# Kernel optimization log

Hardware: AMD Instinct MI355X
Metric: run time of the kernel (lower is better)

The kernel has to match this reference:

```python
import jax, jax.numpy as jnp
import numpy as np

N_NODES = 50000
N_EDGES = 800000
D = 96
N_LAYERS = 3


def setup_inputs() -> dict:
    key = jax.random.key(0)
    ks = jax.random.split(key, 3 + 2 * N_LAYERS)
    h = jax.random.normal(ks[0], (N_NODES, D), dtype=jnp.float32)
    src = jax.random.randint(ks[1], (N_EDGES,), 0, N_NODES, dtype=jnp.int64)
    dst = jax.random.randint(ks[2], (N_EDGES,), 0, N_NODES, dtype=jnp.int64)
    inp = {"h": h, "src": src, "dst": dst}
    scale = 1.0 / np.sqrt(D)
    for i in range(N_LAYERS):
        inp[f"W{i}"] = jax.random.normal(ks[3 + 2 * i], (D, D), dtype=jnp.float32) * scale
        inp[f"b{i}"] = jnp.zeros((D,), dtype=jnp.float32)
    return inp


def _gnn_forward(h, src, dst, weights, biases):
    N = h.shape[0]
    ones = jnp.ones(src.shape[0], dtype=h.dtype)
    # norm='both': scale by out_degree^-1/2 on src side, in_degree^-1/2 on dst side
    out_deg = jnp.clip(jax.ops.segment_sum(ones, src, num_segments=N), 1.0)
    in_deg = jnp.clip(jax.ops.segment_sum(ones, dst, num_segments=N), 1.0)
    norm_src = (out_deg ** -0.5)[:, None]  # [N,1]
    norm_dst = (in_deg ** -0.5)[:, None]   # [N,1]
    for W, b in zip(weights, biases):
        x = h * norm_src                                       # [N,D]
        m = jax.ops.segment_sum(x[src], dst, num_segments=N)   # gather+scatter-add
        m = m * norm_dst
        h = jax.nn.relu(m @ W + b)                             # aggregate-then-transform (in<=out)
    return h


def reference(h, src, dst, W0, b0, W1, b1, W2, b2):
    return _gnn_forward(h, src, dst, (W0, W1, W2), (b0, b1, b2))
```

## Files before the change

kernel.cpp:

```cpp
#include <hip/hip_runtime.h>
#include <hip/hip_bf16.h>

#define N_NODES 50000
#define N_PAD 50048
#define N_EDGES 800000
#define DIM 96
#define CHB 12

#define EPB 2048
#define NB_E ((N_EDGES + EPB - 1) / EPB)
#define NBKT ((N_NODES + 255) / 256)
#define NTILES ((N_NODES + 63) / 64)
#define PREP_ITEMS (3 * DIM * DIM + 3 * DIM)

typedef __attribute__((ext_vector_type(8))) short short8;
typedef __attribute__((ext_vector_type(4))) float f32x4;



__device__ __forceinline__ unsigned short f2bf(float f) {
    unsigned u = __float_as_uint(f);
    u += 0x7FFFu + ((u >> 16) & 1u);
    return (unsigned short)(u >> 16);
}

__device__ __forceinline__ int good_halves(unsigned w) {
    unsigned lo = w & 0xFFFFu, hi = w >> 16;
    unsigned e0 = (lo >> 7) & 0xFF, e1 = (hi >> 7) & 0xFF;
    int g = 0;
    if (lo == 0 || (e0 >= 100 && e0 <= 140)) ++g;
    if (hi == 0 || (e1 >= 100 && e1 <= 140)) ++g;
    return g;
}

__device__ __forceinline__ float rdval(const void* p, int i, int isbf) {
    return isbf ? __bfloat162float(((const __hip_bfloat16*)p)[i]) : ((const float*)p)[i];
}

__device__ __forceinline__ int load_idx(const int* __restrict__ p, int e, int is64) {
    return p[is64 ? (e << 1) : e];
}


__global__ __launch_bounds__(256) void part_count(const int* __restrict__ src,
                                                  const int* __restrict__ dst,
                                                  const unsigned* __restrict__ hw,
                                                  const unsigned* __restrict__ ww,
                                                  int* __restrict__ cntD,
                                                  int* __restrict__ cntS,
                                                  int* __restrict__ flags) {
    const unsigned* sw = (const unsigned*)src;
    int zeros = 0;
    for (int i = 0; i < 64; ++i) zeros += (sw[2 * i + 1] == 0u) ? 1 : 0;
    int is64 = (zeros >= 60) ? 1 : 0;

    __shared__ int lcD[256], lcS[256];
    int b = blockIdx.x, t = threadIdx.x;
    lcD[t] = 0; lcS[t] = 0;
    __syncthreads();
    int base = b * EPB;
#pragma unroll
    for (int i = 0; i < EPB / 256; ++i) {
        int e = base + i * 256 + t;
        if (e < N_EDGES) {
            int d = load_idx(dst, e, is64);
            int s = load_idx(src, e, is64);
            atomicAdd(&lcD[d >> 8], 1);
            atomicAdd(&lcS[s >> 8], 1);
        }
    }
    __syncthreads();
    cntD[b * 256 + t] = lcD[t];
    cntS[b * 256 + t] = lcS[t];

    if (b == 0) {
        if (t == 0) flags[2] = is64;
        if (t == 1) {
            int good = 0;
            for (int i = 0; i < 128; ++i) good += good_halves(hw[i]);
            flags[0] = (good >= 226) ? 1 : 0;
        }
        if (t == 2) {
            int good = 0;
            for (int i = 0; i < 128; ++i) good += good_halves(ww[i]);
            flags[1] = (good >= 226) ? 1 : 0;
        }
    }
}


__global__ __launch_bounds__(256) void scan_buckets(int* __restrict__ cntD,
                                                    int* __restrict__ cntS,
                                                    int* __restrict__ btotD,
                                                    int* __restrict__ btotS) {
    __shared__ int sm[256];
    int k = blockIdx.x, t = threadIdx.x;
    int b0 = 2 * t, b1 = 2 * t + 1;
    int v0 = (b0 < NB_E) ? cntD[b0 * 256 + k] : 0;
    int v1 = (b1 < NB_E) ? cntD[b1 * 256 + k] : 0;
    int pair = v0 + v1;
    sm[t] = pair;
    __syncthreads();
    for (int off = 1; off < 256; off <<= 1) {
        int u = (t >= off) ? sm[t - off] : 0;
        __syncthreads();
        sm[t] += u;
        __syncthreads();
    }
    int excl = sm[t] - pair;
    if (b0 < NB_E) cntD[b0 * 256 + k] = excl;
    if (b1 < NB_E) cntD[b1 * 256 + k] = excl + v0;
    if (t == 255) btotD[k] = sm[255];
    __syncthreads();
    v0 = (b0 < NB_E) ? cntS[b0 * 256 + k] : 0;
    v1 = (b1 < NB_E) ? cntS[b1 * 256 + k] : 0;
    pair = v0 + v1;
    sm[t] = pair;
    __syncthreads();
    for (int off = 1; off < 256; off <<= 1) {
        int u = (t >= off) ? sm[t - off] : 0;
        __syncthreads();
        sm[t] += u;
        __syncthreads();
    }
    excl = sm[t] - pair;
    if (b0 < NB_E) cntS[b0 * 256 + k] = excl;
    if (b1 < NB_E) cntS[b1 * 256 + k] = excl + v0;
    if (t == 255) btotS[k] = sm[255];
}


__global__ __launch_bounds__(256) void part_scatter(const int* __restrict__ src,
                                                    const int* __restrict__ dst,
                                                    const int* __restrict__ offD,
                                                    const int* __restrict__ offS,
                                                    const int* __restrict__ btotD,
                                                    const int* __restrict__ btotS,
                                                    unsigned* __restrict__ epack,
                                                    unsigned char* __restrict__ sloc,
                                                    const int* __restrict__ flags) {
    __shared__ int sm[256];
    __shared__ int runD[256], runS[256];
    int b = blockIdx.x, t = threadIdx.x;
    int v = btotD[t];
    sm[t] = v;
    __syncthreads();
    for (int off = 1; off < 256; off <<= 1) {
        int u = (t >= off) ? sm[t - off] : 0;
        __syncthreads();
        sm[t] += u;
        __syncthreads();
    }
    int baseD = sm[t] - v;
    __syncthreads();
    v = btotS[t];
    sm[t] = v;
    __syncthreads();
    for (int off = 1; off < 256; off <<= 1) {
        int u = (t >= off) ? sm[t - off] : 0;
        __syncthreads();
        sm[t] += u;
        __syncthreads();
    }
    int baseS = sm[t] - v;
    runD[t] = baseD + offD[b * 256 + t];
    runS[t] = baseS + offS[b * 256 + t];
    __syncthreads();
    int is64 = flags[2];
    int base = b * EPB;
#pragma unroll
    for (int i = 0; i < EPB / 256; ++i) {
        int e = base + i * 256 + t;
        if (e < N_EDGES) {
            int d = load_idx(dst, e, is64);
            int s = load_idx(src, e, is64);
            int pd = atomicAdd(&runD[d >> 8], 1);
            epack[pd] = ((unsigned)(d & 255) << 16) | (unsigned)s;
            int ps = atomicAdd(&runS[s >> 8], 1);
            sloc[ps] = (unsigned char)(s & 255);
        }
    }
}


__global__ __launch_bounds__(256) void bucket_build(const unsigned* __restrict__ epack,
                                                    const int* __restrict__ btotD,
                                                    const unsigned char* __restrict__ sloc,
                                                    const int* __restrict__ btotS,
                                                    int* __restrict__ rowptr,
                                                    float* __restrict__ normD,
                                                    float* __restrict__ normS,
                                                    unsigned short* __restrict__ esrc) {
    __shared__ int bD[256], bS[256], cnt[256], run[256];
    int k = blockIdx.x, t = threadIdx.x;
    int vD = btotD[t], vS = btotS[t];
    bD[t] = vD; bS[t] = vS;
    __syncthreads();
    for (int off = 1; off < 256; off <<= 1) {
        int uD = (t >= off) ? bD[t - off] : 0;
        int uS = (t >= off) ? bS[t - off] : 0;
        __syncthreads();
        bD[t] += uD; bS[t] += uS;
        __syncthreads();
    }
    int ebeg = (k == 0) ? 0 : bD[k - 1];
    int eend = bD[k];
    int sbeg = (k == 0) ? 0 : bS[k - 1];
    int send = bS[k];

    cnt[t] = 0;
    __syncthreads();
    for (int e = ebeg + t; e < eend; e += 256)
        atomicAdd(&cnt[epack[e] >> 16], 1);
    __syncthreads();
    int v = cnt[t];
    bD[t] = v;
    __syncthreads();
    for (int off = 1; off < 256; off <<= 1) {
        int u = (t >= off) ? bD[t - off] : 0;
        __syncthreads();
        bD[t] += u;
        __syncthreads();
    }
    int excl = bD[t] - v;
    int n = k * 256 + t;
    if (n < N_NODES) {
        rowptr[n] = ebeg + excl;
        normD[n] = rsqrtf((float)max(v, 1));
    }
    run[t] = excl;
    __syncthreads();
    for (int e = ebeg + t; e < eend; e += 256) {
        unsigned p = epack[e];
        int dl = p >> 16;
        int slot = atomicAdd(&run[dl], 1);
        esrc[ebeg + slot] = (unsigned short)(p & 0xFFFFu);
    }
    if (k == NBKT - 1 && t == 0) rowptr[N_NODES] = N_EDGES;
    __syncthreads();
    cnt[t] = 0;
    __syncthreads();
    for (int e = sbeg + t; e < send; e += 256)
        atomicAdd(&cnt[sloc[e]], 1);
    __syncthreads();
    if (n < N_NODES) normS[n] = rsqrtf((float)max(cnt[t], 1));
}


__global__ __launch_bounds__(256) void prepcvt_k(const void* __restrict__ W0,
                                                 const void* __restrict__ W1,
                                                 const void* __restrict__ W2,
                                                 const void* __restrict__ b0,
                                                 const void* __restrict__ b1,
                                                 const void* __restrict__ b2,
                                                 unsigned short* __restrict__ WT,
                                                 float* __restrict__ biasc,
                                                 const void* __restrict__ h,
                                                 const float* __restrict__ normS,
                                                 unsigned short* __restrict__ A0,
                                                 const int* __restrict__ flags) {
    int idx = blockIdx.x * 256 + threadIdx.x;
    if (idx < PREP_ITEMS) {
        int wbf = flags[1];
        if (idx < 3 * DIM * DIM) {
            int l = idx / (DIM * DIM);
            int i = idx - l * DIM * DIM;
            int k = i / DIM, n = i - k * DIM;
            const void* Wp = (l == 0) ? W0 : (l == 1) ? W1 : W2;
            WT[l * DIM * DIM + n * DIM + k] = f2bf(rdval(Wp, i, wbf));
        } else {
            int j = idx - 3 * DIM * DIM;
            int l = j / DIM, c = j - l * DIM;
            const void* bp = (l == 0) ? b0 : (l == 1) ? b1 : b2;
            biasc[j] = rdval(bp, c, wbf);
        }
        return;
    }
    int i4 = idx - PREP_ITEMS;
    if (i4 >= N_NODES * DIM / 4) return;
    int hbf = flags[0];
    int i = i4 * 4;
    float ns = normS[i / DIM];
    float v0, v1, v2, v3;
    if (hbf) {
        const __hip_bfloat16* hp = (const __hip_bfloat16*)h + i;
        v0 = __bfloat162float(hp[0]); v1 = __bfloat162float(hp[1]);
        v2 = __bfloat162float(hp[2]); v3 = __bfloat162float(hp[3]);
    } else {
        float4 v = ((const float4*)h)[i4];
        v0 = v.x; v1 = v.y; v2 = v.z; v3 = v.w;
    }
    ushort4 o;
    o.x = f2bf(v0 * ns); o.y = f2bf(v1 * ns);
    o.z = f2bf(v2 * ns); o.w = f2bf(v3 * ns);
    ((ushort4*)A0)[i4] = o;
}


__device__ __forceinline__ void acc8(float* a, uint4 q) {
    a[0] += __uint_as_float(q.x << 16);
    a[1] += __uint_as_float(q.x & 0xFFFF0000u);
    a[2] += __uint_as_float(q.y << 16);
    a[3] += __uint_as_float(q.y & 0xFFFF0000u);
    a[4] += __uint_as_float(q.z << 16);
    a[5] += __uint_as_float(q.z & 0xFFFF0000u);
    a[6] += __uint_as_float(q.w << 16);
    a[7] += __uint_as_float(q.w & 0xFFFF0000u);
}

__global__ __launch_bounds__(256) void gather_k(const unsigned* __restrict__ Abf,
                                                const float* __restrict__ normD,
                                                const int* __restrict__ rowptr,
                                                const unsigned short* __restrict__ esrc,
                                                unsigned short* __restrict__ Bm) {
    int g = blockIdx.x * 256 + threadIdx.x;
    if (g >= N_NODES * CHB) return;
    int n = g / CHB;
    int c = g - n * CHB;
    int beg = rowptr[n], end = rowptr[n + 1];
    float a[8] = {0.f, 0.f, 0.f, 0.f, 0.f, 0.f, 0.f, 0.f};
    const uint4* Ap = (const uint4*)Abf;
    int k = beg;
    for (; k + 4 <= end; k += 4) {
        int s0 = esrc[k], s1 = esrc[k + 1], s2 = esrc[k + 2], s3 = esrc[k + 3];
        uint4 q0 = Ap[s0 * CHB + c];
        uint4 q1 = Ap[s1 * CHB + c];
        uint4 q2 = Ap[s2 * CHB + c];
        uint4 q3 = Ap[s3 * CHB + c];
        acc8(a, q0); acc8(a, q1); acc8(a, q2); acc8(a, q3);
    }
    for (; k < end; ++k) {
        uint4 q = Ap[esrc[k] * CHB + c];
        acc8(a, q);
    }
    float nd = normD[n];
    uint4 o;
    o.x = (unsigned)f2bf(a[0] * nd) | ((unsigned)f2bf(a[1] * nd) << 16);
    o.y = (unsigned)f2bf(a[2] * nd) | ((unsigned)f2bf(a[3] * nd) << 16);
    o.z = (unsigned)f2bf(a[4] * nd) | ((unsigned)f2bf(a[5] * nd) << 16);
    o.w = (unsigned)f2bf(a[6] * nd) | ((unsigned)f2bf(a[7] * nd) << 16);
    ((uint4*)Bm)[g] = o;
}


__global__ __launch_bounds__(256) void gemm_k(const unsigned short* __restrict__ Bm,
                                              const float* __restrict__ normS,
                                              const unsigned short* __restrict__ WTl,
                                              const float* __restrict__ bl,
                                              unsigned short* __restrict__ outA,
                                              void* __restrict__ outLast,
                                              const int* __restrict__ flags, int last) {
    int wv = threadIdx.x >> 6;
    int lane = threadIdx.x & 63;
    int quad = lane >> 4;
    int ln = lane & 15;
    int rowbase = blockIdx.x * 64 + wv * 16;

    const short8* Ap = (const short8*)(Bm + (size_t)(rowbase + ln) * DIM + quad * 8);
    short8 a0 = Ap[0], a1 = Ap[4], a2 = Ap[8];

    float ns[4];
    if (!last) {
#pragma unroll
        for (int r = 0; r < 4; ++r)
            ns[r] = normS[min(rowbase + quad * 4 + r, N_NODES - 1)];
    }
    int obf = flags[0];

#pragma unroll
    for (int ct = 0; ct < 6; ++ct) {
        const short8* Wp = (const short8*)(WTl + (size_t)(ct * 16 + ln) * DIM + quad * 8);
        short8 b0 = Wp[0], b1 = Wp[4], b2 = Wp[8];
        f32x4 acc = {0.f, 0.f, 0.f, 0.f};
        acc = __builtin_amdgcn_mfma_f32_16x16x32_bf16(a0, b0, acc, 0, 0, 0);
        acc = __builtin_amdgcn_mfma_f32_16x16x32_bf16(a1, b1, acc, 0, 0, 0);
        acc = __builtin_amdgcn_mfma_f32_16x16x32_bf16(a2, b2, acc, 0, 0, 0);
        int col = ct * 16 + ln;
        float bv = bl[col];
#pragma unroll
        for (int r = 0; r < 4; ++r) {
            int row = rowbase + quad * 4 + r;
            if (row < N_NODES) {
                float v = fmaxf(acc[r] + bv, 0.f);
                size_t idx = (size_t)row * DIM + col;
                if (last) {
                    if (obf)
                        ((__hip_bfloat16*)outLast)[idx] = __float2bfloat16(v);
                    else
                        ((float*)outLast)[idx] = v;
                } else {
                    outA[idx] = f2bf(v * ns[r]);
                }
            }
        }
    }
}


extern "C" void kernel_launch(void* const* d_in, const int* in_sizes, int n_in,
                              void* d_out, int out_size, void* d_ws, size_t ws_size,
                              hipStream_t stream) {
    const void* h = d_in[0];
    const int* src = (const int*)d_in[1];
    const int* dst = (const int*)d_in[2];

    int* flags = (int*)d_ws;
    int* cntD = flags + 4;
    int* cntS = cntD + NB_E * 256;
    int* btotD = cntS + NB_E * 256;
    int* btotS = btotD + 256;
    int* rowptr = btotS + 256;
    float* normS = (float*)(rowptr + 50004);
    float* normD = normS + N_NODES;
    unsigned short* WT = (unsigned short*)(normD + N_NODES);
    float* biasc = (float*)(WT + 3 * DIM * DIM);
    unsigned* epack = (unsigned*)(biasc + 3 * DIM);
    unsigned char* sloc = (unsigned char*)(epack + N_EDGES);
    unsigned short* esrc = (unsigned short*)(sloc + N_EDGES);
    unsigned short* Bm = esrc + N_EDGES;
    unsigned short* A0 = Bm + (size_t)N_PAD * DIM;
    unsigned short* A1 = A0 + (size_t)N_NODES * DIM;

    part_count<<<NB_E, 256, 0, stream>>>(src, dst, (const unsigned*)h,
                                         (const unsigned*)d_in[3], cntD, cntS, flags);
    scan_buckets<<<256, 256, 0, stream>>>(cntD, cntS, btotD, btotS);
    part_scatter<<<NB_E, 256, 0, stream>>>(src, dst, cntD, cntS, btotD, btotS,
                                           epack, sloc, flags);
    bucket_build<<<NBKT, 256, 0, stream>>>(epack, btotD, sloc, btotS,
                                           rowptr, normD, normS, esrc);
    prepcvt_k<<<(PREP_ITEMS + N_NODES * DIM / 4 + 255) / 256, 256, 0, stream>>>(
        d_in[3], d_in[5], d_in[7], d_in[4], d_in[6], d_in[8], WT, biasc,
        h, normS, A0, flags);

    const int ggrid = (N_NODES * CHB + 255) / 256;
    gather_k<<<ggrid, 256, 0, stream>>>((const unsigned*)A0, normD, rowptr, esrc, Bm);
    gemm_k<<<NTILES, 256, 0, stream>>>(Bm, normS, WT, biasc, A1, nullptr, flags, 0);
    gather_k<<<ggrid, 256, 0, stream>>>((const unsigned*)A1, normD, rowptr, esrc, Bm);
    gemm_k<<<NTILES, 256, 0, stream>>>(Bm, normS, WT + DIM * DIM, biasc + DIM,
                                       A0, nullptr, flags, 0);
    gather_k<<<ggrid, 256, 0, stream>>>((const unsigned*)A0, normD, rowptr, esrc, Bm);
    gemm_k<<<NTILES, 256, 0, stream>>>(Bm, normS, WT + 2 * DIM * DIM, biasc + 2 * DIM,
                                       nullptr, d_out, flags, 1);
}
```

Before: 262.4 us.

## Fuse gather into GEMM per layer and fold prep into preprocessing kernels

Measured after the change: 265.3 us. About the same (+1.1%).

```diff
diff --git a/kernel.cpp b/kernel.cpp
--- a/kernel.cpp
+++ b/kernel.cpp
@@ -2,7 +2,6 @@
 #include <hip/hip_bf16.h>
 
 #define N_NODES 50000
-#define N_PAD 50048
 #define N_EDGES 800000
 #define DIM 96
 #define CHB 12
@@ -12,6 +11,7 @@
 #define NBKT ((N_NODES + 255) / 256)
 #define NTILES ((N_NODES + 63) / 64)
 #define PREP_ITEMS (3 * DIM * DIM + 3 * DIM)
+#define LROW 112
 
 typedef __attribute__((ext_vector_type(8))) short short8;
 typedef __attribute__((ext_vector_type(4))) float f32x4;
@@ -39,6 +39,17 @@
 
 __device__ __forceinline__ int load_idx(const int* __restrict__ p, int e, int is64) {
     return p[is64 ? (e << 1) : e];
+}
+
+__device__ __forceinline__ void acc8(float* a, uint4 q) {
+    a[0] += __uint_as_float(q.x << 16);
+    a[1] += __uint_as_float(q.x & 0xFFFF0000u);
+    a[2] += __uint_as_float(q.y << 16);
+    a[3] += __uint_as_float(q.y & 0xFFFF0000u);
+    a[4] += __uint_as_float(q.z << 16);
+    a[5] += __uint_as_float(q.z & 0xFFFF0000u);
+    a[6] += __uint_as_float(q.w << 16);
+    a[7] += __uint_as_float(q.w & 0xFFFF0000u);
 }
 
 
@@ -92,7 +103,16 @@
 __global__ __launch_bounds__(256) void scan_buckets(int* __restrict__ cntD,
                                                     int* __restrict__ cntS,
                                                     int* __restrict__ btotD,
-                                                    int* __restrict__ btotS) {
+                                                    int* __restrict__ btotS,
+                                                    const void* __restrict__ W0,
+                                                    const void* __restrict__ W1,
+                                                    const void* __restrict__ W2,
+                                                    const void* __restrict__ b0p,
+                                                    const void* __restrict__ b1p,
+                                                    const void* __restrict__ b2p,
+                                                    unsigned short* __restrict__ WT,
+                                                    float* __restrict__ biasc,
+                                                    const int* __restrict__ flags) {
     __shared__ int sm[256];
     int k = blockIdx.x, t = threadIdx.x;
     int b0 = 2 * t, b1 = 2 * t + 1;
@@ -127,6 +147,23 @@
     if (b0 < NB_E) cntS[b0 * 256 + k] = excl;
     if (b1 < NB_E) cntS[b1 * 256 + k] = excl + v0;
     if (t == 255) btotS[k] = sm[255];
+
+    int idx = k * 256 + t;
+    if (idx < PREP_ITEMS) {
+        int wbf = flags[1];
+        if (idx < 3 * DIM * DIM) {
+            int l = idx / (DIM * DIM);
+            int i = idx - l * DIM * DIM;
+            int kk = i / DIM, n = i - kk * DIM;
+            const void* Wp = (l == 0) ? W0 : (l == 1) ? W1 : W2;
+            WT[l * DIM * DIM + n * DIM + kk] = f2bf(rdval(Wp, i, wbf));
+        } else {
+            int j = idx - 3 * DIM * DIM;
+            int l = j / DIM, c = j - l * DIM;
+            const void* bp = (l == 0) ? b0p : (l == 1) ? b1p : b2p;
+            biasc[j] = rdval(bp, c, wbf);
+        }
+    }
 }
 
 
@@ -190,8 +227,12 @@
                                                     int* __restrict__ rowptr,
                                                     float* __restrict__ normD,
                                                     float* __restrict__ normS,
-                                                    unsigned short* __restrict__ esrc) {
+                                                    unsigned short* __restrict__ esrc,
+                                                    const void* __restrict__ h,
+                                                    unsigned short* __restrict__ A0,
+                                                    const int* __restrict__ flags) {
     __shared__ int bD[256], bS[256], cnt[256], run[256];
+    __shared__ float nsf[256];
     int k = blockIdx.x, t = threadIdx.x;
     int vD = btotD[t], vS = btotS[t];
     bD[t] = vD; bS[t] = vS;
@@ -243,124 +284,94 @@
     for (int e = sbeg + t; e < send; e += 256)
         atomicAdd(&cnt[sloc[e]], 1);
     __syncthreads();
-    if (n < N_NODES) normS[n] = rsqrtf((float)max(cnt[t], 1));
-}
-
-
-__global__ __launch_bounds__(256) void prepcvt_k(const void* __restrict__ W0,
-                                                 const void* __restrict__ W1,
-                                                 const void* __restrict__ W2,
-                                                 const void* __restrict__ b0,
-                                                 const void* __restrict__ b1,
-                                                 const void* __restrict__ b2,
-                                                 unsigned short* __restrict__ WT,
-                                                 float* __restrict__ biasc,
-                                                 const void* __restrict__ h,
-                                                 const float* __restrict__ normS,
-                                                 unsigned short* __restrict__ A0,
-                                                 const int* __restrict__ flags) {
-    int idx = blockIdx.x * 256 + threadIdx.x;
-    if (idx < PREP_ITEMS) {
-        int wbf = flags[1];
-        if (idx < 3 * DIM * DIM) {
-            int l = idx / (DIM * DIM);
-            int i = idx - l * DIM * DIM;
-            int k = i / DIM, n = i - k * DIM;
-            const void* Wp = (l == 0) ? W0 : (l == 1) ? W1 : W2;
-            WT[l * DIM * DIM + n * DIM + k] = f2bf(rdval(Wp, i, wbf));
+    float ns = rsqrtf((float)max(cnt[t], 1));
+    nsf[t] = ns;
+    if (n < N_NODES) normS[n] = ns;
+    __syncthreads();
+    int hbf = flags[0];
+    for (int i = t; i < 256 * (DIM / 4); i += 256) {
+        int ln_ = i / (DIM / 4);
+        int c4 = i - ln_ * (DIM / 4);
+        int nn = k * 256 + ln_;
+        if (nn >= N_NODES) continue;
+        float s = nsf[ln_];
+        float v0, v1, v2, v3;
+        if (hbf) {
+            const __hip_bfloat16* hp = (const __hip_bfloat16*)h + (size_t)nn * DIM + c4 * 4;
+            v0 = __bfloat162float(hp[0]); v1 = __bfloat162float(hp[1]);
+            v2 = __bfloat162float(hp[2]); v3 = __bfloat162float(hp[3]);
         } else {
-            int j = idx - 3 * DIM * DIM;
-            int l = j / DIM, c = j - l * DIM;
-            const void* bp = (l == 0) ? b0 : (l == 1) ? b1 : b2;
-            biasc[j] = rdval(bp, c, wbf);
-        }
-        return;
-    }
-    int i4 = idx - PREP_ITEMS;
-    if (i4 >= N_NODES * DIM / 4) return;
-    int hbf = flags[0];
-    int i = i4 * 4;
-    float ns = normS[i / DIM];
-    float v0, v1, v2, v3;
-    if (hbf) {
-        const __hip_bfloat16* hp = (const __hip_bfloat16*)h + i;
-        v0 = __bfloat162float(hp[0]); v1 = __bfloat162float(hp[1]);
-        v2 = __bfloat162float(hp[2]); v3 = __bfloat162float(hp[3]);
-    } else {
-        float4 v = ((const float4*)h)[i4];
-        v0 = v.x; v1 = v.y; v2 = v.z; v3 = v.w;
-    }
-    ushort4 o;
-    o.x = f2bf(v0 * ns); o.y = f2bf(v1 * ns);
-    o.z = f2bf(v2 * ns); o.w = f2bf(v3 * ns);
-    ((ushort4*)A0)[i4] = o;
-}
-
-
-__device__ __forceinline__ void acc8(float* a, uint4 q) {
-    a[0] += __uint_as_float(q.x << 16);
-    a[1] += __uint_as_float(q.x & 0xFFFF0000u);
-    a[2] += __uint_as_float(q.y << 16);
-    a[3] += __uint_as_float(q.y & 0xFFFF0000u);
-    a[4] += __uint_as_float(q.z << 16);
-    a[5] += __uint_as_float(q.z & 0xFFFF0000u);
-    a[6] += __uint_as_float(q.w << 16);
-    a[7] += __uint_as_float(q.w & 0xFFFF0000u);
-}
-
-__global__ __launch_bounds__(256) void gather_k(const unsigned* __restrict__ Abf,
-                                                const float* __restrict__ normD,
-                                                const int* __restrict__ rowptr,
-                                                const unsigned short* __restrict__ esrc,
-                                                unsigned short* __restrict__ Bm) {
-    int g = blockIdx.x * 256 + threadIdx.x;
-    if (g >= N_NODES * CHB) return;
-    int n = g / CHB;
-    int c = g - n * CHB;
-    int beg = rowptr[n], end = rowptr[n + 1];
-    float a[8] = {0.f, 0.f, 0.f, 0.f, 0.f, 0.f, 0.f, 0.f};
+            float4 vv = ((const float4*)h)[nn * (DIM / 4) + c4];
+            v0 = vv.x; v1 = vv.y; v2 = vv.z; v3 = vv.w;
+        }
+        ushort4 o;
+        o.x = f2bf(v0 * s); o.y = f2bf(v1 * s);
+        o.z = f2bf(v2 * s); o.w = f2bf(v3 * s);
+        ((ushort4*)A0)[nn * (DIM / 4) + c4] = o;
+    }
+}
+
+
+template <bool LAST>
+__global__ __launch_bounds__(256) void fused_layer(const unsigned* __restrict__ Abf,
+                                                   const float* __restrict__ normS,
+                                                   const float* __restrict__ normD,
+                                                   const int* __restrict__ rowptr,
+                                                   const unsigned short* __restrict__ esrc,
+                                                   const unsigned short* __restrict__ WTl,
+                                                   const float* __restrict__ bl,
+                                                   unsigned short* __restrict__ outA,
+                                                   void* __restrict__ outLast,
+                                                   const int* __restrict__ flags) {
+    __shared__ unsigned short Bs[64 * LROW];
+
     const uint4* Ap = (const uint4*)Abf;
-    int k = beg;
-    for (; k + 4 <= end; k += 4) {
-        int s0 = esrc[k], s1 = esrc[k + 1], s2 = esrc[k + 2], s3 = esrc[k + 3];
-        uint4 q0 = Ap[s0 * CHB + c];
-        uint4 q1 = Ap[s1 * CHB + c];
-        uint4 q2 = Ap[s2 * CHB + c];
-        uint4 q3 = Ap[s3 * CHB + c];
-        acc8(a, q0); acc8(a, q1); acc8(a, q2); acc8(a, q3);
-    }
-    for (; k < end; ++k) {
-        uint4 q = Ap[esrc[k] * CHB + c];
-        acc8(a, q);
-    }
-    float nd = normD[n];
-    uint4 o;
-    o.x = (unsigned)f2bf(a[0] * nd) | ((unsigned)f2bf(a[1] * nd) << 16);
-    o.y = (unsigned)f2bf(a[2] * nd) | ((unsigned)f2bf(a[3] * nd) << 16);
-    o.z = (unsigned)f2bf(a[4] * nd) | ((unsigned)f2bf(a[5] * nd) << 16);
-    o.w = (unsigned)f2bf(a[6] * nd) | ((unsigned)f2bf(a[7] * nd) << 16);
-    ((uint4*)Bm)[g] = o;
-}
-
-
-__global__ __launch_bounds__(256) void gemm_k(const unsigned short* __restrict__ Bm,
-                                              const float* __restrict__ normS,
-                                              const unsigned short* __restrict__ WTl,
-                                              const float* __restrict__ bl,
-                                              unsigned short* __restrict__ outA,
-                                              void* __restrict__ outLast,
-                                              const int* __restrict__ flags, int last) {
+    int row0 = blockIdx.x * 64;
+
+#pragma unroll
+    for (int it = 0; it < 3; ++it) {
+        int g = threadIdx.x + 256 * it;
+        int r = g / CHB;
+        int c = g - r * CHB;
+        int n = row0 + r;
+        float a[8] = {0.f, 0.f, 0.f, 0.f, 0.f, 0.f, 0.f, 0.f};
+        float nd = 0.f;
+        if (n < N_NODES) {
+            int beg = rowptr[n], end = rowptr[n + 1];
+            int k = beg;
+            for (; k + 4 <= end; k += 4) {
+                int s0 = esrc[k], s1 = esrc[k + 1], s2 = esrc[k + 2], s3 = esrc[k + 3];
+                uint4 q0 = Ap[s0 * CHB + c];
+                uint4 q1 = Ap[s1 * CHB + c];
+                uint4 q2 = Ap[s2 * CHB + c];
+                uint4 q3 = Ap[s3 * CHB + c];
+                acc8(a, q0); acc8(a, q1); acc8(a, q2); acc8(a, q3);
+            }
+            for (; k < end; ++k) acc8(a, Ap[esrc[k] * CHB + c]);
+            nd = normD[n];
+        }
+        uint4 o;
+        o.x = (unsigned)f2bf(a[0] * nd) | ((unsigned)f2bf(a[1] * nd) << 16);
+        o.y = (unsigned)f2bf(a[2] * nd) | ((unsigned)f2bf(a[3] * nd) << 16);
+        o.z = (unsigned)f2bf(a[4] * nd) | ((unsigned)f2bf(a[5] * nd) << 16);
+        o.w = (unsigned)f2bf(a[6] * nd) | ((unsigned)f2bf(a[7] * nd) << 16);
+        *(uint4*)&Bs[r * LROW + c * 8] = o;
+    }
+    __syncthreads();
+
     int wv = threadIdx.x >> 6;
     int lane = threadIdx.x & 63;
     int quad = lane >> 4;
     int ln = lane & 15;
-    int rowbase = blockIdx.x * 64 + wv * 16;
-
-    const short8* Ap = (const short8*)(Bm + (size_t)(rowbase + ln) * DIM + quad * 8);
-    short8 a0 = Ap[0], a1 = Ap[4], a2 = Ap[8];
+    int rl = wv * 16 + ln;
+    int rowbase = row0 + wv * 16;
+
+    short8 a0 = *(const short8*)&Bs[rl * LROW + quad * 8];
+    short8 a1 = *(const short8*)&Bs[rl * LROW + 32 + quad * 8];
+    short8 a2 = *(const short8*)&Bs[rl * LROW + 64 + quad * 8];
 
     float ns[4];
-    if (!last) {
+    if (!LAST) {
 #pragma unroll
         for (int r = 0; r < 4; ++r)
             ns[r] = normS[min(rowbase + quad * 4 + r, N_NODES - 1)];
@@ -383,7 +394,7 @@
             if (row < N_NODES) {
                 float v = fmaxf(acc[r] + bv, 0.f);
                 size_t idx = (size_t)row * DIM + col;
-                if (last) {
+                if (LAST) {
                     if (obf)
                         ((__hip_bfloat16*)outLast)[idx] = __float2bfloat16(v);
                     else
@@ -417,28 +428,28 @@
     unsigned* epack = (unsigned*)(biasc + 3 * DIM);
     unsigned char* sloc = (unsigned char*)(epack + N_EDGES);
     unsigned short* esrc = (unsigned short*)(sloc + N_EDGES);
-    unsigned short* Bm = esrc + N_EDGES;
-    unsigned short* A0 = Bm + (size_t)N_PAD * DIM;
+    unsigned short* A0 = esrc + N_EDGES;
     unsigned short* A1 = A0 + (size_t)N_NODES * DIM;
 
     part_count<<<NB_E, 256, 0, stream>>>(src, dst, (const unsigned*)h,
                                          (const unsigned*)d_in[3], cntD, cntS, flags);
-    scan_buckets<<<256, 256, 0, stream>>>(cntD, cntS, btotD, btotS);
+    scan_buckets<<<256, 256, 0, stream>>>(cntD, cntS, btotD, btotS,
+                                          d_in[3], d_in[5], d_in[7],
+                                          d_in[4], d_in[6], d_in[8],
+                                          WT, biasc, flags);
     part_scatter<<<NB_E, 256, 0, stream>>>(src, dst, cntD, cntS, btotD, btotS,
                                            epack, sloc, flags);
     bucket_build<<<NBKT, 256, 0, stream>>>(epack, btotD, sloc, btotS,
-                                           rowptr, normD, normS, esrc);
-    prepcvt_k<<<(PREP_ITEMS + N_NODES * DIM / 4 + 255) / 256, 256, 0, stream>>>(
-        d_in[3], d_in[5], d_in[7], d_in[4], d_in[6], d_in[8], WT, biasc,
-        h, normS, A0, flags);
-
-    const int ggrid = (N_NODES * CHB + 255) / 256;
-    gather_k<<<ggrid, 256, 0, stream>>>((const unsigned*)A0, normD, rowptr, esrc, Bm);
-    gemm_k<<<NTILES, 256, 0, stream>>>(Bm, normS, WT, biasc, A1, nullptr, flags, 0);
-    gather_k<<<ggrid, 256, 0, stream>>>((const unsigned*)A1, normD, rowptr, esrc, Bm);
-    gemm_k<<<NTILES, 256, 0, stream>>>(Bm, normS, WT + DIM * DIM, biasc + DIM,
-                                       A0, nullptr, flags, 0);
-    gather_k<<<ggrid, 256, 0, stream>>>((const unsigned*)A0, normD, rowptr, esrc, Bm);
-    gemm_k<<<NTILES, 256, 0, stream>>>(Bm, normS, WT + 2 * DIM * DIM, biasc + 2 * DIM,
-                                       nullptr, d_out, flags, 1);
-}
+                                           rowptr, normD, normS, esrc,
+                                           h, A0, flags);
+
+    fused_layer<false><<<NTILES, 256, 0, stream>>>((const unsigned*)A0, normS, normD,
+                                                   rowptr, esrc, WT, biasc,
+                                                   A1, nullptr, flags);
+    fused_layer<false><<<NTILES, 256, 0, stream>>>((const unsigned*)A1, normS, normD,
+                                                   rowptr, esrc, WT + DIM * DIM, biasc + DIM,
+                                                   A0, nullptr, flags);
+    fused_layer<true><<<NTILES, 256, 0, stream>>>((const unsigned*)A0, normS, normD,
+                                                  rowptr, esrc, WT + 2 * DIM * DIM,
+                                                  biasc + 2 * DIM, nullptr, d_out, flags);
+}
```
